# Kernel optimization log

Measured on AMD Instinct MI355X. Metric: run time of the kernel, lower is better.

Reference implementation:

```python
import jax, jax.numpy as jnp
import numpy as np

IN_FEATURES = 512
NUM_CASES = 64
N_POINTS = 131072
HIDDEN = 512
OUT_FEATURES = 512


def _wn_linear(x, V, g, b):
    # torch weight_norm with dim=0 on Linear weight [out, in]: per-row norm over in-dim
    W = V * (g / jnp.linalg.norm(V, axis=1))[:, None]
    return x @ W.T + b


def _consolidative_matmul(mask, x):
    # group-by-caseID mean pooling expressed as masked matmul (matches torch forward)
    sel_sum = jnp.sum(mask, axis=-1, keepdims=True)
    sel_sum = jnp.maximum(sel_sum, 1.0)  # relu(s-1)+1 == max(s,1) for s>=0
    return (mask @ x) / sel_sum


def setup_inputs() -> dict:
    key = jax.random.key(0)
    ks = jax.random.split(key, 8)
    feat = jax.random.normal(ks[0], (N_POINTS, IN_FEATURES), dtype=jnp.float32)
    cid = jax.random.randint(ks[1], (N_POINTS, 1), 0, NUM_CASES).astype(jnp.float32)
    x = jnp.concatenate([feat, cid], axis=-1)  # [N, 513]
    s = 0.05
    V0 = jax.random.normal(ks[2], (HIDDEN, IN_FEATURES), dtype=jnp.float32) * s
    g0 = jnp.ones((HIDDEN,), dtype=jnp.float32)
    b0 = jnp.zeros((HIDDEN,), dtype=jnp.float32)
    V1 = jax.random.normal(ks[3], (HIDDEN, HIDDEN), dtype=jnp.float32) * s
    g1 = jnp.ones((HIDDEN,), dtype=jnp.float32)
    b1 = jnp.zeros((HIDDEN,), dtype=jnp.float32)
    Wf = jax.random.normal(ks[4], (OUT_FEATURES, HIDDEN), dtype=jnp.float32) * s
    bf = jnp.zeros((OUT_FEATURES,), dtype=jnp.float32)
    return {"x": x, "V0": V0, "g0": g0, "b0": b0,
            "V1": V1, "g1": g1, "b1": b1, "Wf": Wf, "bf": bf}


def reference(x, V0, g0, b0, V1, g1, b1, Wf, bf):
    feat = x[..., :IN_FEATURES]                    # [N, 512]
    cid = jax.lax.stop_gradient(x[..., IN_FEATURES:IN_FEATURES + 1])  # [N, 1]
    case_range = jnp.arange(NUM_CASES, dtype=x.dtype)[:, None]        # [C, 1]
    d = jnp.swapaxes(cid, -1, -2) - case_range     # [C, N]
    # Unit_function: 1 iff -0.5 < d < 0.5, else 0 (hard, zero-grad)
    mask = jnp.where((d > -0.5) & (d < 0.5), 1.0, 0.0).astype(x.dtype)
    mask = jax.lax.stop_gradient(mask)
    h = _consolidative_matmul(mask, feat)          # [C, 512] per-case mean
    h = jax.nn.silu(_wn_linear(h, V0, g0, b0))
    h = jax.nn.silu(_wn_linear(h, V1, g1, b1))
    h = h @ Wf.T + bf                              # final layer, identity activation
    out = jnp.swapaxes(mask, -1, -2) @ h           # scatter-back combine [N, 512]
    return out
```

## Files before the change

kernel.cpp:

```cpp
#include <hip/hip_runtime.h>
#include <math.h>

#define NPTS   131072
#define INF    512
#define ROWF   513
#define NCASE  64
#define HID    512
#define NB     256
#define CHUNK  512
#define SEG    16

typedef float v4f __attribute__((ext_vector_type(4)));

__global__ __launch_bounds__(256)
void k_hist(const float* __restrict__ x, int* __restrict__ hist,
            int* __restrict__ cids) {
  __shared__ int h[NCASE];
  const int t = threadIdx.x;
  const int b = blockIdx.x;
  if (t < NCASE) h[t] = 0;
  __syncthreads();
  const int base = b * CHUNK;
  for (int i = t; i < CHUNK; i += 256) {
    float cf = x[(size_t)(base + i) * ROWF + INF];
    int c = (int)(cf + 0.5f);
    cids[base + i] = c;
    atomicAdd(&h[c], 1);
  }
  __syncthreads();
  if (t < NCASE) hist[t * NB + b] = h[t];
}

__global__ __launch_bounds__(256)
void k_scan(const int* __restrict__ hist, int* __restrict__ rel,
            int* __restrict__ cnt) {
  __shared__ int buf[NB];
  const int c = blockIdx.x;
  const int t = threadIdx.x;
  const int v = hist[c * NB + t];
  buf[t] = v;
  __syncthreads();
  for (int d = 1; d < NB; d <<= 1) {
    int u = (t >= d) ? buf[t - d] : 0;
    __syncthreads();
    buf[t] += u;
    __syncthreads();
  }
  rel[t * NCASE + c] = buf[t] - v;
  if (t == NB - 1) cnt[c] = buf[t];
}

__global__ __launch_bounds__(64)
void k_build(const int* __restrict__ cids, const int* __restrict__ rel,
             const int* __restrict__ cnt, int* __restrict__ idxlist) {
  __shared__ int cidl[CHUNK];
  const int lane = threadIdx.x;
  const int b = blockIdx.x;
  for (int i = lane; i < CHUNK; i += 64) cidl[i] = cids[b * CHUNK + i];
  int lv = cnt[lane];
  int sc = lv;
  for (int d = 1; d < 64; d <<= 1) {
    int u = __shfl_up(sc, d, 64);
    if (lane >= d) sc += u;
  }
  const int base = sc - lv;
  __syncthreads();
  int myoff = rel[b * NCASE + lane] + base;
  int rank = 0;
  for (int i = 0; i < CHUNK; ++i) {
    if (cidl[i] == lane) { idxlist[myoff + rank] = b * CHUNK + i; ++rank; }
  }
}

__global__ __launch_bounds__(128)
void k_sum(const float* __restrict__ x, const int* __restrict__ idxlist,
           const int* __restrict__ cnt, float* __restrict__ psum) {
  __shared__ float buf[2][HID];
  const int t = threadIdx.x;
  const int lane = t & 63;
  const int w = t >> 6;
  const int s = blockIdx.x;
  const int c = blockIdx.y;

  int lv = cnt[lane];
  int sc = lv;
  for (int d = 1; d < 64; d <<= 1) {
    int u = __shfl_up(sc, d, 64);
    if (lane >= d) sc += u;
  }
  const int bs = __shfl(sc - lv, c, 64);
  const int n  = __shfl(lv, c, 64);

  const int p0 = (s * n) / SEG;
  const int p1 = ((s + 1) * n) / SEG;
  const int m  = p1 - p0;

  float a[8];
  #pragma unroll
  for (int k = 0; k < 8; ++k) a[k] = 0.f;

  for (int j0 = w * 64; j0 < m; j0 += 128) {
    const int nb = (m - j0 < 64) ? (m - j0) : 64;
    int iv = (lane < nb) ? idxlist[bs + p0 + j0 + lane] : 0;
    int jj = 0;
    for (; jj + 4 <= nb; jj += 4) {
      float v[4][8];
      #pragma unroll
      for (int u = 0; u < 4; ++u) {
        int idx = __shfl(iv, jj + u, 64);
        const float* r = x + (size_t)idx * ROWF + lane;
        #pragma unroll
        for (int k = 0; k < 8; ++k) v[u][k] = __builtin_nontemporal_load(r + 64 * k);
      }
      #pragma unroll
      for (int u = 0; u < 4; ++u) {
        #pragma unroll
        for (int k = 0; k < 8; ++k) a[k] += v[u][k];
      }
    }
    for (; jj < nb; ++jj) {
      int idx = __shfl(iv, jj, 64);
      const float* r = x + (size_t)idx * ROWF + lane;
      #pragma unroll
      for (int k = 0; k < 8; ++k) a[k] += __builtin_nontemporal_load(r + 64 * k);
    }
  }

  #pragma unroll
  for (int k = 0; k < 8; ++k) buf[w][lane + 64 * k] = a[k];
  __syncthreads();
  float* od = psum + ((size_t)c * SEG + s) * HID;
  for (int f = t; f < HID; f += 128) od[f] = buf[0][f] + buf[1][f];
}

__global__ __launch_bounds__(256)
void k_scale2(const float* __restrict__ V0, const float* __restrict__ g0,
              const float* __restrict__ V1, const float* __restrict__ g1,
              float* __restrict__ scale0, float* __restrict__ scale1) {
  __shared__ float red[256];
  const int row = blockIdx.x;
  const int t   = threadIdx.x;
  const bool first = row < 512;
  const int r = first ? row : row - 512;
  const float* vr = (first ? V0 : V1) + (size_t)r * HID;
  float s = 0.f;
  for (int k = t; k < HID; k += 256) { float v = vr[k]; s += v * v; }
  red[t] = s;
  __syncthreads();
  for (int w = 128; w > 0; w >>= 1) {
    if (t < w) red[t] += red[t + w];
    __syncthreads();
  }
  if (t == 0) {
    float g = first ? g0[r] : g1[r];
    (first ? scale0 : scale1)[r] = g / sqrtf(red[0]);
  }
}

template <bool SILU, bool SCALED, bool REDUCE>
__global__ __launch_bounds__(256)
void k_layer(const float* __restrict__ hin, const float* __restrict__ W,
             const float* __restrict__ scale, const float* __restrict__ bias,
             const int* __restrict__ cnt, float* __restrict__ hout) {
  __shared__ float hrow[HID];
  const int n = blockIdx.y;
  const int t = threadIdx.x;
  const int o = blockIdx.x * 256 + t;
  if (REDUCE) {
    float inv = 1.f / fmaxf((float)cnt[n], 1.f);
    for (int f = t; f < HID; f += 256) {
      float s = 0.f;
      for (int seg = 0; seg < SEG; ++seg)
        s += hin[((size_t)n * SEG + seg) * HID + f];
      hrow[f] = s * inv;
    }
  } else {
    for (int f = t; f < HID; f += 256) hrow[f] = hin[(size_t)n * HID + f];
  }
  __syncthreads();
  const float* wr = W + (size_t)o * HID;
  float s0 = 0.f, s1 = 0.f, s2 = 0.f, s3 = 0.f;
  for (int k = 0; k < HID; k += 4) {
    float4 h4 = *(const float4*)&hrow[k];
    float4 w4 = *(const float4*)&wr[k];
    s0 += h4.x * w4.x; s1 += h4.y * w4.y;
    s2 += h4.z * w4.z; s3 += h4.w * w4.w;
  }
  float sdot = (s0 + s1) + (s2 + s3);
  float y = SCALED ? (sdot * scale[o] + bias[o]) : (sdot + bias[o]);
  if (SILU) y = y / (1.f + expf(-y));
  hout[(size_t)n * HID + o] = y;
}

__global__ __launch_bounds__(256)
void k_scatter(const int* __restrict__ cids, const float* __restrict__ h3,
               float* __restrict__ out) {
  __shared__ int cl[128];
  const int t = threadIdx.x;
  const int q = t & 127;
  const int half = t >> 7;
  const int base = blockIdx.x * 128;
  if (t < 128) cl[t] = cids[base + t];
  __syncthreads();
  #pragma unroll 8
  for (int p = half; p < 128; p += 2) {
    int c = cl[p];
    v4f hv = ((const v4f*)(h3 + (size_t)c * HID))[q];
    v4f* dst = (v4f*)(out + (size_t)(base + p) * HID) + q;
    __builtin_nontemporal_store(hv, dst);
  }
}

extern "C" void kernel_launch(void* const* d_in, const int* in_sizes, int n_in,
                              void* d_out, int out_size, void* d_ws, size_t ws_size,
                              hipStream_t stream) {
  const float* x  = (const float*)d_in[0];
  const float* V0 = (const float*)d_in[1];
  const float* g0 = (const float*)d_in[2];
  const float* b0 = (const float*)d_in[3];
  const float* V1 = (const float*)d_in[4];
  const float* g1 = (const float*)d_in[5];
  const float* b1 = (const float*)d_in[6];
  const float* Wf = (const float*)d_in[7];
  const float* bf = (const float*)d_in[8];
  float* out = (float*)d_out;
  float* ws  = (float*)d_ws;

  size_t off = 0;
  float* psum   = ws + off; off += (size_t)NCASE * SEG * HID;
  float* h1     = ws + off; off += NCASE * HID;
  float* h2     = ws + off; off += NCASE * HID;
  float* h3     = ws + off; off += NCASE * HID;
  float* scale0 = ws + off; off += 512;
  float* scale1 = ws + off; off += 512;
  int* iws = (int*)(ws + off);
  size_t ioff = 0;
  int* hist    = iws + ioff; ioff += NCASE * NB;
  int* rel     = iws + ioff; ioff += NB * NCASE;
  int* cnt     = iws + ioff; ioff += NCASE;
  int* cids    = iws + ioff; ioff += NPTS;
  int* idxlist = iws + ioff; ioff += NPTS;

  k_scale2<<<dim3(1024), dim3(256), 0, stream>>>(V0, g0, V1, g1, scale0, scale1);
  k_hist  <<<dim3(NB), dim3(256), 0, stream>>>(x, hist, cids);
  k_scan  <<<dim3(NCASE), dim3(NB), 0, stream>>>(hist, rel, cnt);
  k_build <<<dim3(NB), dim3(64), 0, stream>>>(cids, rel, cnt, idxlist);
  k_sum   <<<dim3(SEG, NCASE), dim3(128), 0, stream>>>(x, idxlist, cnt, psum);
  k_layer<true,  true,  true ><<<dim3(2, NCASE), dim3(256), 0, stream>>>(psum, V0, scale0, b0, cnt, h1);
  k_layer<true,  true,  false><<<dim3(2, NCASE), dim3(256), 0, stream>>>(h1,   V1, scale1, b1, cnt, h2);
  k_layer<false, false, false><<<dim3(2, NCASE), dim3(256), 0, stream>>>(h2,   Wf, nullptr, bf, cnt, h3);
  k_scatter<<<dim3(NPTS / 128), dim3(256), 0, stream>>>(cids, h3, out);
}
```

Measured before the change: 200.0 us.

## Replace gather-based case pooling with streaming per-block LDS accumulation

Removes the histogram, scan, index-list build and gathered segment-sum kernels. Instead, each block streams a contiguous chunk of rows and accumulates per-case sums in a 64x512 shared-memory array, then writes block partials that a new reduction kernel sums and normalizes. This avoids random row gathers and several launches, but adds a large partial-sum buffer write and read, and relies on a 128KB LDS allocation that limits occupancy to one block per CU.

After: 191.5 us. -4.2%, faster.

```diff
diff --git a/kernel.cpp b/kernel.cpp
--- a/kernel.cpp
+++ b/kernel.cpp
@@ -8,129 +8,85 @@
 #define HID    512
 #define NB     256
 #define CHUNK  512
-#define SEG    16
 
 typedef float v4f __attribute__((ext_vector_type(4)));
 
-__global__ __launch_bounds__(256)
-void k_hist(const float* __restrict__ x, int* __restrict__ hist,
-            int* __restrict__ cids) {
-  __shared__ int h[NCASE];
+__global__ __launch_bounds__(512)
+void k_stream(const float* __restrict__ x, float* __restrict__ psum,
+              float* __restrict__ pcnt, int* __restrict__ cids) {
+  __shared__ float acc[NCASE * HID];
+  __shared__ int   cidl[CHUNK];
+  __shared__ int   cnth[NCASE];
   const int t = threadIdx.x;
   const int b = blockIdx.x;
-  if (t < NCASE) h[t] = 0;
+  const int base = b * CHUNK;
+
+  for (int i = t; i < NCASE * HID; i += 512) acc[i] = 0.f;
+  if (t < NCASE) cnth[t] = 0;
   __syncthreads();
-  const int base = b * CHUNK;
-  for (int i = t; i < CHUNK; i += 256) {
-    float cf = x[(size_t)(base + i) * ROWF + INF];
+
+  {
+    float cf = x[(size_t)(base + t) * ROWF + INF];
     int c = (int)(cf + 0.5f);
-    cids[base + i] = c;
-    atomicAdd(&h[c], 1);
+    cidl[t] = c;
+    cids[base + t] = c;
+    atomicAdd(&cnth[c], 1);
   }
   __syncthreads();
-  if (t < NCASE) hist[t * NB + b] = h[t];
-}
 
-__global__ __launch_bounds__(256)
-void k_scan(const int* __restrict__ hist, int* __restrict__ rel,
-            int* __restrict__ cnt) {
-  __shared__ int buf[NB];
-  const int c = blockIdx.x;
-  const int t = threadIdx.x;
-  const int v = hist[c * NB + t];
-  buf[t] = v;
+  const int f = t;
+  const float* xp = x + (size_t)base * ROWF + f;
+
+  float v[8];
+  #pragma unroll
+  for (int j = 0; j < 8; ++j)
+    v[j] = __builtin_nontemporal_load(xp + (size_t)j * ROWF);
+
+  for (int p = 0; p < CHUNK; p += 8) {
+    float nv[8];
+    if (p + 8 < CHUNK) {
+      #pragma unroll
+      for (int j = 0; j < 8; ++j)
+        nv[j] = __builtin_nontemporal_load(xp + (size_t)(p + 8 + j) * ROWF);
+    }
+    int cj[8];
+    #pragma unroll
+    for (int j = 0; j < 8; ++j) cj[j] = cidl[p + j];
+    #pragma unroll
+    for (int j = 0; j < 8; ++j) acc[cj[j] * HID + f] += v[j];
+    #pragma unroll
+    for (int j = 0; j < 8; ++j) v[j] = nv[j];
+  }
   __syncthreads();
-  for (int d = 1; d < NB; d <<= 1) {
-    int u = (t >= d) ? buf[t - d] : 0;
-    __syncthreads();
-    buf[t] += u;
-    __syncthreads();
-  }
-  rel[t * NCASE + c] = buf[t] - v;
-  if (t == NB - 1) cnt[c] = buf[t];
-}
 
-__global__ __launch_bounds__(64)
-void k_build(const int* __restrict__ cids, const int* __restrict__ rel,
-             const int* __restrict__ cnt, int* __restrict__ idxlist) {
-  __shared__ int cidl[CHUNK];
-  const int lane = threadIdx.x;
-  const int b = blockIdx.x;
-  for (int i = lane; i < CHUNK; i += 64) cidl[i] = cids[b * CHUNK + i];
-  int lv = cnt[lane];
-  int sc = lv;
-  for (int d = 1; d < 64; d <<= 1) {
-    int u = __shfl_up(sc, d, 64);
-    if (lane >= d) sc += u;
-  }
-  const int base = sc - lv;
-  __syncthreads();
-  int myoff = rel[b * NCASE + lane] + base;
-  int rank = 0;
-  for (int i = 0; i < CHUNK; ++i) {
-    if (cidl[i] == lane) { idxlist[myoff + rank] = b * CHUNK + i; ++rank; }
-  }
+  float* od = psum + (size_t)b * NCASE * HID;
+  for (int c = 0; c < NCASE; ++c)
+    __builtin_nontemporal_store(acc[c * HID + f], &od[c * HID + f]);
+  if (t < NCASE) pcnt[b * NCASE + t] = (float)cnth[t];
 }
 
 __global__ __launch_bounds__(128)
-void k_sum(const float* __restrict__ x, const int* __restrict__ idxlist,
-           const int* __restrict__ cnt, float* __restrict__ psum) {
-  __shared__ float buf[2][HID];
-  const int t = threadIdx.x;
-  const int lane = t & 63;
-  const int w = t >> 6;
-  const int s = blockIdx.x;
-  const int c = blockIdx.y;
+void k_h0(const float* __restrict__ psum, const float* __restrict__ pcnt,
+          float* __restrict__ h0) {
+  __shared__ float cs[128];
+  const int c  = blockIdx.x;
+  const int fq = blockIdx.y;
+  const int t  = threadIdx.x;
+  const int f  = fq * 128 + t;
 
-  int lv = cnt[lane];
-  int sc = lv;
-  for (int d = 1; d < 64; d <<= 1) {
-    int u = __shfl_up(sc, d, 64);
-    if (lane >= d) sc += u;
+  const float* p = psum + (size_t)c * HID + f;
+  float s = 0.f;
+  #pragma unroll 8
+  for (int b = 0; b < NB; ++b) s += p[(size_t)b * NCASE * HID];
+
+  cs[t] = pcnt[t * NCASE + c] + pcnt[(t + 128) * NCASE + c];
+  __syncthreads();
+  for (int w = 64; w > 0; w >>= 1) {
+    if (t < w) cs[t] += cs[t + w];
+    __syncthreads();
   }
-  const int bs = __shfl(sc - lv, c, 64);
-  const int n  = __shfl(lv, c, 64);
-
-  const int p0 = (s * n) / SEG;
-  const int p1 = ((s + 1) * n) / SEG;
-  const int m  = p1 - p0;
-
-  float a[8];
-  #pragma unroll
-  for (int k = 0; k < 8; ++k) a[k] = 0.f;
-
-  for (int j0 = w * 64; j0 < m; j0 += 128) {
-    const int nb = (m - j0 < 64) ? (m - j0) : 64;
-    int iv = (lane < nb) ? idxlist[bs + p0 + j0 + lane] : 0;
-    int jj = 0;
-    for (; jj + 4 <= nb; jj += 4) {
-      float v[4][8];
-      #pragma unroll
-      for (int u = 0; u < 4; ++u) {
-        int idx = __shfl(iv, jj + u, 64);
-        const float* r = x + (size_t)idx * ROWF + lane;
-        #pragma unroll
-        for (int k = 0; k < 8; ++k) v[u][k] = __builtin_nontemporal_load(r + 64 * k);
-      }
-      #pragma unroll
-      for (int u = 0; u < 4; ++u) {
-        #pragma unroll
-        for (int k = 0; k < 8; ++k) a[k] += v[u][k];
-      }
-    }
-    for (; jj < nb; ++jj) {
-      int idx = __shfl(iv, jj, 64);
-      const float* r = x + (size_t)idx * ROWF + lane;
-      #pragma unroll
-      for (int k = 0; k < 8; ++k) a[k] += __builtin_nontemporal_load(r + 64 * k);
-    }
-  }
-
-  #pragma unroll
-  for (int k = 0; k < 8; ++k) buf[w][lane + 64 * k] = a[k];
-  __syncthreads();
-  float* od = psum + ((size_t)c * SEG + s) * HID;
-  for (int f = t; f < HID; f += 128) od[f] = buf[0][f] + buf[1][f];
+  float cnt = fmaxf(cs[0], 1.f);
+  h0[(size_t)c * HID + f] = s / cnt;
 }
 
 __global__ __launch_bounds__(256)
@@ -157,26 +113,16 @@
   }
 }
 
-template <bool SILU, bool SCALED, bool REDUCE>
+template <bool SILU, bool SCALED>
 __global__ __launch_bounds__(256)
 void k_layer(const float* __restrict__ hin, const float* __restrict__ W,
              const float* __restrict__ scale, const float* __restrict__ bias,
-             const int* __restrict__ cnt, float* __restrict__ hout) {
+             float* __restrict__ hout) {
   __shared__ float hrow[HID];
   const int n = blockIdx.y;
   const int t = threadIdx.x;
   const int o = blockIdx.x * 256 + t;
-  if (REDUCE) {
-    float inv = 1.f / fmaxf((float)cnt[n], 1.f);
-    for (int f = t; f < HID; f += 256) {
-      float s = 0.f;
-      for (int seg = 0; seg < SEG; ++seg)
-        s += hin[((size_t)n * SEG + seg) * HID + f];
-      hrow[f] = s * inv;
-    }
-  } else {
-    for (int f = t; f < HID; f += 256) hrow[f] = hin[(size_t)n * HID + f];
-  }
+  for (int f = t; f < HID; f += 256) hrow[f] = hin[(size_t)n * HID + f];
   __syncthreads();
   const float* wr = W + (size_t)o * HID;
   float s0 = 0.f, s1 = 0.f, s2 = 0.f, s3 = 0.f;
@@ -227,27 +173,21 @@
   float* ws  = (float*)d_ws;
 
   size_t off = 0;
-  float* psum   = ws + off; off += (size_t)NCASE * SEG * HID;
+  float* psum   = ws + off; off += (size_t)NB * NCASE * HID;
+  float* pcnt   = ws + off; off += NB * NCASE;
+  float* h0     = ws + off; off += NCASE * HID;
   float* h1     = ws + off; off += NCASE * HID;
   float* h2     = ws + off; off += NCASE * HID;
   float* h3     = ws + off; off += NCASE * HID;
   float* scale0 = ws + off; off += 512;
   float* scale1 = ws + off; off += 512;
-  int* iws = (int*)(ws + off);
-  size_t ioff = 0;
-  int* hist    = iws + ioff; ioff += NCASE * NB;
-  int* rel     = iws + ioff; ioff += NB * NCASE;
-  int* cnt     = iws + ioff; ioff += NCASE;
-  int* cids    = iws + ioff; ioff += NPTS;
-  int* idxlist = iws + ioff; ioff += NPTS;
+  int*   cids   = (int*)(ws + off); off += NPTS;
 
   k_scale2<<<dim3(1024), dim3(256), 0, stream>>>(V0, g0, V1, g1, scale0, scale1);
-  k_hist  <<<dim3(NB), dim3(256), 0, stream>>>(x, hist, cids);
-  k_scan  <<<dim3(NCASE), dim3(NB), 0, stream>>>(hist, rel, cnt);
-  k_build <<<dim3(NB), dim3(64), 0, stream>>>(cids, rel, cnt, idxlist);
-  k_sum   <<<dim3(SEG, NCASE), dim3(128), 0, stream>>>(x, idxlist, cnt, psum);
-  k_layer<true,  true,  true ><<<dim3(2, NCASE), dim3(256), 0, stream>>>(psum, V0, scale0, b0, cnt, h1);
-  k_layer<true,  true,  false><<<dim3(2, NCASE), dim3(256), 0, stream>>>(h1,   V1, scale1, b1, cnt, h2);
-  k_layer<false, false, false><<<dim3(2, NCASE), dim3(256), 0, stream>>>(h2,   Wf, nullptr, bf, cnt, h3);
+  k_stream<<<dim3(NB), dim3(512), 0, stream>>>(x, psum, pcnt, cids);
+  k_h0    <<<dim3(NCASE, 4), dim3(128), 0, stream>>>(psum, pcnt, h0);
+  k_layer<true,  true ><<<dim3(2, NCASE), dim3(256), 0, stream>>>(h0, V0, scale0, b0, h1);
+  k_layer<true,  true ><<<dim3(2, NCASE), dim3(256), 0, stream>>>(h1, V1, scale1, b1, h2);
+  k_layer<false, false><<<dim3(2, NCASE), dim3(256), 0, stream>>>(h2, Wf, nullptr, bf, h3);
   k_scatter<<<dim3(NPTS / 128), dim3(256), 0, stream>>>(cids, h3, out);
 }
```
